# Kernel optimization log

Measured on AMD Instinct MI355X. Metric: run time of the kernel, lower is better.

Reference implementation:

```python
import jax, jax.numpy as jnp
import numpy as np

N, E, IN, H, L, G, C = 100000, 600000, 64, 128, 3, 256, 10
EPS_BN = 1e-5


def _tconv(x, src, dst, Wq, bq, Wk, bk, Wv, bv, Ws, bs):
    # PyG TransformerConv, heads=1: per-edge dot-product attention softmaxed over
    # in-neighbors of each target node, plus root (skip) linear.
    n = x.shape[0]
    q = x @ Wq + bq                      # [N,H]
    k = x @ Wk + bk                      # [N,H]
    v = x @ Wv + bv                      # [N,H]
    scale = 1.0 / jnp.sqrt(jnp.asarray(q.shape[-1], x.dtype))
    a = jnp.sum(q[dst] * k[src], axis=-1) * scale          # [E]
    m = jax.ops.segment_max(a, dst, num_segments=n)         # per-target max
    ex = jnp.exp(a - m[dst])
    s = jax.ops.segment_sum(ex, dst, num_segments=n)
    w = ex / s[dst]                                          # softmax over edges per target
    agg = jax.ops.segment_sum(v[src] * w[:, None], dst, num_segments=n)  # [N,H]
    return agg + x @ Ws + bs


def _bn(x, g, b):
    # BatchNorm1d, training mode: biased batch variance, eps=1e-5
    mu = jnp.mean(x, axis=0)
    var = jnp.mean((x - mu) ** 2, axis=0)
    return (x - mu) * jax.lax.rsqrt(var + EPS_BN) * g + b


def setup_inputs():
    key = jax.random.key(0)
    ks = jax.random.split(key, 40)
    sc = 0.05
    inp = {
        "x": jax.random.normal(ks[0], (N, IN), dtype=jnp.float32),
        "edge_index": jax.random.randint(ks[1], (2, E), 0, N, dtype=jnp.int32),
        "batch": jnp.sort(jax.random.randint(ks[2], (N,), 0, G, dtype=jnp.int32)),
        # conv1: input_dim -> hidden
        "Wq1": jax.random.normal(ks[3], (IN, H)) * sc,
        "bq1": jnp.zeros((H,), jnp.float32),
        "Wk1": jax.random.normal(ks[4], (IN, H)) * sc,
        "bk1": jnp.zeros((H,), jnp.float32),
        "Wv1": jax.random.normal(ks[5], (IN, H)) * sc,
        "bv1": jnp.zeros((H,), jnp.float32),
        "Ws1": jax.random.normal(ks[6], (IN, H)) * sc,
        "bs1": jnp.zeros((H,), jnp.float32),
        "bn1_g": jnp.ones((H,), jnp.float32),
        "bn1_b": jnp.zeros((H,), jnp.float32),
        # stacked hidden layers: hidden -> hidden
        "Wq": jax.random.normal(ks[7], (L, H, H)) * sc,
        "bq": jnp.zeros((L, H), jnp.float32),
        "Wk": jax.random.normal(ks[8], (L, H, H)) * sc,
        "bk": jnp.zeros((L, H), jnp.float32),
        "Wv": jax.random.normal(ks[9], (L, H, H)) * sc,
        "bv": jnp.zeros((L, H), jnp.float32),
        "Ws": jax.random.normal(ks[10], (L, H, H)) * sc,
        "bs": jnp.zeros((L, H), jnp.float32),
        "bn_g": jnp.ones((L, H), jnp.float32),
        "bn_b": jnp.zeros((L, H), jnp.float32),
        # classifier head
        "lin_W": jax.random.normal(ks[11], (H, C)) * sc,
        "lin_b": jnp.zeros((C,), jnp.float32),
    }
    return inp


def reference(x, edge_index, batch, Wq1, bq1, Wk1, bk1, Wv1, bv1, Ws1, bs1,
              bn1_g, bn1_b, Wq, bq, Wk, bk, Wv, bv, Ws, bs, bn_g, bn_b,
              lin_W, lin_b):
    src, dst = edge_index[0], edge_index[1]
    h = _tconv(x, src, dst, Wq1, bq1, Wk1, bk1, Wv1, bv1, Ws1, bs1)
    h = jax.nn.relu(_bn(h, bn1_g, bn1_b))
    for i in range(L):
        h = _tconv(h, src, dst, Wq[i], bq[i], Wk[i], bk[i], Wv[i], bv[i], Ws[i], bs[i])
        h = jax.nn.relu(_bn(h, bn_g[i], bn_b[i]))
    # global_mean_pool over graphs
    sums = jax.ops.segment_sum(h, batch, num_segments=G)          # [G,H]
    cnts = jax.ops.segment_sum(jnp.ones((h.shape[0],), h.dtype), batch, num_segments=G)
    pooled = sums / jnp.maximum(cnts, 1.0)[:, None]
    return pooled @ lin_W + lin_b                                  # [G,C]
```

## Files before the change

kernel.cpp:

```cpp
#include <hip/hip_runtime.h>
#include <hip/hip_bf16.h>

#define IN_DIM 64
#define H_DIM 128
#define L_LAYERS 3
#define G_GRAPHS 256
#define C_CLASSES 10

typedef short bf16x8 __attribute__((ext_vector_type(8)));
typedef float f32x4 __attribute__((ext_vector_type(4)));

__device__ inline unsigned short bf16rne(float x) {
    unsigned v = __float_as_uint(x);
    v += 0x7FFFu + ((v >> 16) & 1u);
    return (unsigned short)(v >> 16);
}

__device__ inline void bsplit(float x, unsigned short& h, unsigned short& l) {
    h = bf16rne(x);
    float hf = __uint_as_float((unsigned)h << 16);
    l = bf16rne(x - hf);
}

__global__ void count_deg(const int* __restrict__ dst, int* __restrict__ deg,
                          int* __restrict__ erank, int e) {
    int i = blockIdx.x * blockDim.x + threadIdx.x;
    if (i < e) erank[i] = atomicAdd(&deg[dst[i]], 1);
}

__global__ __launch_bounds__(256) void scan1(const int* __restrict__ deg,
                                             int* __restrict__ rowptr,
                                             int* __restrict__ bsum, int n) {
    int i = blockIdx.x * 256 + threadIdx.x;
    int v = (i < n) ? deg[i] : 0;
    __shared__ int sm[256];
    sm[threadIdx.x] = v;
    __syncthreads();
    for (int off = 1; off < 256; off <<= 1) {
        int x = (threadIdx.x >= off) ? sm[threadIdx.x - off] : 0;
        __syncthreads();
        sm[threadIdx.x] += x;
        __syncthreads();
    }
    if (i < n) rowptr[i + 1] = sm[threadIdx.x];
    if (threadIdx.x == 255) bsum[blockIdx.x] = sm[255];
}

__global__ __launch_bounds__(512) void scan2(int* __restrict__ bsum, int nblk) {
    __shared__ int sm[512];
    int t = threadIdx.x;
    int v = (t < nblk) ? bsum[t] : 0;
    sm[t] = v;
    __syncthreads();
    for (int off = 1; off < 512; off <<= 1) {
        int x = (t >= off) ? sm[t - off] : 0;
        __syncthreads();
        sm[t] += x;
        __syncthreads();
    }
    if (t < nblk) bsum[t] = sm[t] - v;
}

__global__ void scan3(int* __restrict__ rowptr, const int* __restrict__ bsum, int n) {
    int i = blockIdx.x * 256 + threadIdx.x;
    if (i < n) rowptr[i + 1] += bsum[i >> 8];
    if (i == 0) rowptr[0] = 0;
}

__global__ void scatter_edges(const int* __restrict__ src, const int* __restrict__ dst,
                              const int* __restrict__ rowptr, const int* __restrict__ erank,
                              int* __restrict__ esrc, int e) {
    int i = blockIdx.x * blockDim.x + threadIdx.x;
    if (i < e) esrc[rowptr[dst[i]] + erank[i]] = src[i];
}

template <int K, bool BN>
__global__ __launch_bounds__(256) void prep_x(const float* __restrict__ X, int nrows,
                                              int rows_pad,
                                              const float* __restrict__ bnsc,
                                              const float* __restrict__ bnsh,
                                              unsigned short* __restrict__ XF) {
    const int GPR = K / 8;
    int e8 = blockIdx.x * 256 + threadIdx.x;
    int row = e8 / GPR;
    int k0 = (e8 - row * GPR) * 8;
    if (row >= rows_pad) return;
    float v[8];
    if (row < nrows) {
        float4 a = *(const float4*)(X + (size_t)row * K + k0);
        float4 b = *(const float4*)(X + (size_t)row * K + k0 + 4);
        v[0] = a.x; v[1] = a.y; v[2] = a.z; v[3] = a.w;
        v[4] = b.x; v[5] = b.y; v[6] = b.z; v[7] = b.w;
        if (BN) {
            float4 s0 = *(const float4*)(bnsc + k0);
            float4 s1 = *(const float4*)(bnsc + k0 + 4);
            float4 h0 = *(const float4*)(bnsh + k0);
            float4 h1 = *(const float4*)(bnsh + k0 + 4);
            v[0] = fmaxf(0.f, fmaf(v[0], s0.x, h0.x));
            v[1] = fmaxf(0.f, fmaf(v[1], s0.y, h0.y));
            v[2] = fmaxf(0.f, fmaf(v[2], s0.z, h0.z));
            v[3] = fmaxf(0.f, fmaf(v[3], s0.w, h0.w));
            v[4] = fmaxf(0.f, fmaf(v[4], s1.x, h1.x));
            v[5] = fmaxf(0.f, fmaf(v[5], s1.y, h1.y));
            v[6] = fmaxf(0.f, fmaf(v[6], s1.z, h1.z));
            v[7] = fmaxf(0.f, fmaf(v[7], s1.w, h1.w));
        }
    } else {
#pragma unroll
        for (int j = 0; j < 8; ++j) v[j] = 0.f;
    }
    unsigned short h[8], l[8];
#pragma unroll
    for (int j = 0; j < 8; ++j) bsplit(v[j], h[j], l[j]);
    size_t f = (size_t)(row >> 4) * (K >> 5) + (k0 >> 5);
    int lane = ((k0 >> 3) & 3) * 16 + (row & 15);
    unsigned short* p = XF + f * 1024 + lane * 8;
    uint4 hv, lv;
    hv.x = h[0] | (h[1] << 16); hv.y = h[2] | (h[3] << 16);
    hv.z = h[4] | (h[5] << 16); hv.w = h[6] | (h[7] << 16);
    lv.x = l[0] | (l[1] << 16); lv.y = l[2] | (l[3] << 16);
    lv.z = l[4] | (l[5] << 16); lv.w = l[6] | (l[7] << 16);
    *(uint4*)p = hv;
    *(uint4*)(p + 512) = lv;
}

template <int K>
__global__ __launch_bounds__(256) void prep_w(const float* __restrict__ W0,
                                              const float* __restrict__ W1,
                                              const float* __restrict__ W2,
                                              const float* __restrict__ W3,
                                              unsigned short* __restrict__ WF) {
    const float* W;
    switch (blockIdx.y) {
        case 0:  W = W0; break;
        case 1:  W = W1; break;
        case 2:  W = W2; break;
        default: W = W3; break;
    }
    const int GPC = K / 8;
    int e8 = blockIdx.x * 256 + threadIdx.x;
    if (e8 >= K * 16) return;
    int col = e8 / GPC;
    int k0 = (e8 - col * GPC) * 8;
    float v[8];
#pragma unroll
    for (int j = 0; j < 8; ++j) v[j] = W[(size_t)(k0 + j) * 128 + col];
    unsigned short h[8], l[8];
#pragma unroll
    for (int j = 0; j < 8; ++j) bsplit(v[j], h[j], l[j]);
    size_t f = (size_t)(col >> 4) * (K >> 5) + (k0 >> 5);
    int lane = ((k0 >> 3) & 3) * 16 + (col & 15);
    const size_t wstride = (size_t)8 * (K >> 5) * 1024;
    unsigned short* p = WF + blockIdx.y * wstride + f * 1024 + lane * 8;
    uint4 hv, lv;
    hv.x = h[0] | (h[1] << 16); hv.y = h[2] | (h[3] << 16);
    hv.z = h[4] | (h[5] << 16); hv.w = h[6] | (h[7] << 16);
    lv.x = l[0] | (l[1] << 16); lv.y = l[2] | (l[3] << 16);
    lv.z = l[4] | (l[5] << 16); lv.w = l[6] | (l[7] << 16);
    *(uint4*)p = hv;
    *(uint4*)(p + 512) = lv;
}

template <int K>
__global__ __launch_bounds__(256) void gemm_mfma(
    const unsigned short* __restrict__ XF, const unsigned short* __restrict__ WF,
    int n, int strips,
    const float* __restrict__ b0, const float* __restrict__ b1,
    const float* __restrict__ b2, const float* __restrict__ b3,
    float* __restrict__ oq, unsigned short* __restrict__ ok,
    unsigned short* __restrict__ ov, float* __restrict__ oskip) {
    constexpr int KB = K >> 5;
    int wid = (blockIdx.x * 256 + threadIdx.x) >> 6;
    int l = threadIdx.x & 63;
    if (wid >= strips) return;

    bf16x8 A[2][KB][2];
#pragma unroll
    for (int mf = 0; mf < 2; ++mf)
#pragma unroll
        for (int kb = 0; kb < KB; ++kb) {
            const unsigned short* p =
                XF + ((size_t)(wid * 2 + mf) * KB + kb) * 1024 + l * 8;
            A[mf][kb][0] = *(const bf16x8*)p;
            A[mf][kb][1] = *(const bf16x8*)(p + 512);
        }

    const int rbase = wid * 32 + ((l >> 4) << 2);
#pragma unroll
    for (int nf = 0; nf < 8; ++nf) {
        const int col = nf * 16 + (l & 15);
#pragma unroll
        for (int y = 0; y < 4; ++y) {
            const float* bias = (y == 0) ? b0 : (y == 1) ? b1 : (y == 2) ? b2 : b3;
            const unsigned short* WFy = WF + (size_t)y * (8 * KB * 1024);
            bf16x8 B[KB][2];
#pragma unroll
            for (int kb = 0; kb < KB; ++kb) {
                const unsigned short* p = WFy + ((size_t)(nf * KB + kb)) * 1024 + l * 8;
                B[kb][0] = *(const bf16x8*)p;
                B[kb][1] = *(const bf16x8*)(p + 512);
            }
            f32x4 acc[2];
            acc[0] = (f32x4){0.f, 0.f, 0.f, 0.f};
            acc[1] = (f32x4){0.f, 0.f, 0.f, 0.f};
#pragma unroll
            for (int kb = 0; kb < KB; ++kb) {
#pragma unroll
                for (int mf = 0; mf < 2; ++mf) {
                    acc[mf] = __builtin_amdgcn_mfma_f32_16x16x32_bf16(
                        A[mf][kb][0], B[kb][0], acc[mf], 0, 0, 0);
                    acc[mf] = __builtin_amdgcn_mfma_f32_16x16x32_bf16(
                        A[mf][kb][0], B[kb][1], acc[mf], 0, 0, 0);
                    acc[mf] = __builtin_amdgcn_mfma_f32_16x16x32_bf16(
                        A[mf][kb][1], B[kb][0], acc[mf], 0, 0, 0);
                }
            }
            float bb = bias[col];
            if (y == 0 || y == 3) {
                float* outp = (y == 0) ? oq : oskip;
#pragma unroll
                for (int mf = 0; mf < 2; ++mf)
#pragma unroll
                    for (int r = 0; r < 4; ++r) {
                        int row = rbase + mf * 16 + r;
                        if (row < n) outp[(size_t)row * 128 + col] = acc[mf][r] + bb;
                    }
            } else {
                unsigned short* outp = (y == 1) ? ok : ov;
#pragma unroll
                for (int mf = 0; mf < 2; ++mf)
#pragma unroll
                    for (int r = 0; r < 4; ++r) {
                        int row = rbase + mf * 16 + r;
                        if (row < n) outp[(size_t)row * 128 + col] = bf16rne(acc[mf][r] + bb);
                    }
            }
        }
    }
}

__global__ __launch_bounds__(256) void attn_kernel(
    const float* __restrict__ q, const unsigned short* __restrict__ k16,
    const unsigned short* __restrict__ v16,
    const int* __restrict__ rowptr, const int* __restrict__ esrc,
    float* __restrict__ h2, int n) {
    int wid = (blockIdx.x * blockDim.x + threadIdx.x) >> 6;
    int lane = threadIdx.x & 63;
    if (wid >= n) return;
    int f0 = lane * 2;
    float2 qv = *(const float2*)(q + (size_t)wid * 128 + f0);
    const float scale = 0.08838834764831845f;
    int beg = rowptr[wid], end = rowptr[wid + 1];
    if (beg == end) return;
    float m = -3.402823466e38f, ssum = 0.f, acc0 = 0.f, acc1 = 0.f;

    unsigned kA[4], vA[4];
#pragma unroll
    for (int c = 0; c < 4; ++c) {
        int jj = beg + c; jj = jj < end ? jj : end - 1;
        int s = esrc[jj];
        kA[c] = *(const unsigned*)(k16 + (size_t)s * 128 + f0);
        vA[c] = *(const unsigned*)(v16 + (size_t)s * 128 + f0);
    }
    for (int j = beg; j < end; j += 4) {
        unsigned kB[4], vB[4];
        if (j + 4 < end) {
#pragma unroll
            for (int c = 0; c < 4; ++c) {
                int jj = j + 4 + c; jj = jj < end ? jj : end - 1;
                int s = esrc[jj];
                kB[c] = *(const unsigned*)(k16 + (size_t)s * 128 + f0);
                vB[c] = *(const unsigned*)(v16 + (size_t)s * 128 + f0);
            }
        } else {
#pragma unroll
            for (int c = 0; c < 4; ++c) { kB[c] = 0; vB[c] = 0; }
        }
        int cnt = end - j;
#pragma unroll
        for (int c = 0; c < 4; ++c) {
            if (c < cnt) {
                unsigned kw = kA[c], vw = vA[c];
                float kx = __uint_as_float(kw << 16);
                float ky = __uint_as_float(kw & 0xFFFF0000u);
                float d = qv.x * kx + qv.y * ky;
#pragma unroll
                for (int off = 32; off; off >>= 1) d += __shfl_xor(d, off);
                d *= scale;
                if (d > m) {
                    float r = __expf(m - d);
                    ssum *= r; acc0 *= r; acc1 *= r; m = d;
                }
                float w = __expf(d - m);
                ssum += w;
                acc0 += w * __uint_as_float(vw << 16);
                acc1 += w * __uint_as_float(vw & 0xFFFF0000u);
            }
        }
#pragma unroll
        for (int c = 0; c < 4; ++c) { kA[c] = kB[c]; vA[c] = vB[c]; }
    }
    float inv = 1.f / ssum;
    float2* o = (float2*)(h2 + (size_t)wid * 128 + f0);
    float2 cur = *o;
    cur.x += acc0 * inv;
    cur.y += acc1 * inv;
    *o = cur;
}

__global__ __launch_bounds__(256) void bn_stats(const float* __restrict__ h2,
                                                float* __restrict__ psum,
                                                float* __restrict__ psq, int n) {
    int f = threadIdx.x & 127;
    int rp = threadIdx.x >> 7;
    float s = 0.f, s2 = 0.f;
    for (int r = blockIdx.x * 2 + rp; r < n; r += gridDim.x * 2) {
        float x = h2[(size_t)r * 128 + f];
        s += x;
        s2 += x * x;
    }
    __shared__ float sm[256], sm2[256];
    sm[threadIdx.x] = s;
    sm2[threadIdx.x] = s2;
    __syncthreads();
    if (rp == 0) {
        psum[blockIdx.x * 128 + f] = sm[f] + sm[128 + f];
        psq[blockIdx.x * 128 + f] = sm2[f] + sm2[128 + f];
    }
}

__global__ __launch_bounds__(512) void bn_finalize(const float* __restrict__ psum,
                                                   const float* __restrict__ psq,
                                                   const float* __restrict__ g,
                                                   const float* __restrict__ b,
                                                   float* __restrict__ scale,
                                                   float* __restrict__ shift, int n) {
    int f = threadIdx.x & 127, part = threadIdx.x >> 7;
    float s = 0.f, s2 = 0.f;
#pragma unroll 4
    for (int i = part; i < 256; i += 4) {
        s += psum[i * 128 + f];
        s2 += psq[i * 128 + f];
    }
    __shared__ float sa[512], sb[512];
    sa[threadIdx.x] = s;
    sb[threadIdx.x] = s2;
    __syncthreads();
    if (part == 0) {
        s = sa[f] + sa[128 + f] + sa[256 + f] + sa[384 + f];
        s2 = sb[f] + sb[128 + f] + sb[256 + f] + sb[384 + f];
        float inv_n = 1.f / (float)n;
        float mu = s * inv_n;
        float var = s2 * inv_n - mu * mu;
        float sc = g[f] * rsqrtf(var + 1e-5f);
        scale[f] = sc;
        shift[f] = b[f] - mu * sc;
    }
}

__global__ __launch_bounds__(256) void pool_kernel(const float* __restrict__ h,
                                                   const float* __restrict__ bnsc,
                                                   const float* __restrict__ bnsh,
                                                   const int* __restrict__ batch,
                                                   float* __restrict__ pooled, int n) {
    int g = blockIdx.x;
    int lo = 0, hi = n;
    while (lo < hi) { int mid = (lo + hi) >> 1; if (batch[mid] < g) lo = mid + 1; else hi = mid; }
    int start = lo;
    lo = start; hi = n;
    while (lo < hi) { int mid = (lo + hi) >> 1; if (batch[mid] < g + 1) lo = mid + 1; else hi = mid; }
    int end = lo;
    int f = threadIdx.x & 127, rp = threadIdx.x >> 7;
    float sc = bnsc[f], sh = bnsh[f];
    float s = 0.f;
    for (int r = start + rp; r < end; r += 2)
        s += fmaxf(0.f, fmaf(h[(size_t)r * 128 + f], sc, sh));
    __shared__ float sm[256];
    sm[threadIdx.x] = s;
    __syncthreads();
    if (rp == 0) {
        float tot = sm[f] + sm[128 + f];
        float cnt = (float)(end - start);
        pooled[g * 128 + f] = tot / fmaxf(cnt, 1.f);
    }
}

__global__ void head_kernel(const float* __restrict__ pooled, const float* __restrict__ W,
                            const float* __restrict__ bias, float* __restrict__ out) {
    int g = blockIdx.x;
    int lane = threadIdx.x;
    float p0 = pooled[g * 128 + lane];
    float p1 = pooled[g * 128 + 64 + lane];
#pragma unroll
    for (int c = 0; c < C_CLASSES; ++c) {
        float d = p0 * W[lane * C_CLASSES + c] + p1 * W[(64 + lane) * C_CLASSES + c];
#pragma unroll
        for (int off = 32; off; off >>= 1) d += __shfl_xor(d, off);
        if (lane == 0) out[g * C_CLASSES + c] = d + bias[c];
    }
}

extern "C" void kernel_launch(void* const* d_in, const int* in_sizes, int n_in,
                              void* d_out, int out_size, void* d_ws, size_t ws_size,
                              hipStream_t stream) {
    const int N = in_sizes[0] / IN_DIM;
    const int E = in_sizes[1] / 2;

    const float* x     = (const float*)d_in[0];
    const int* ei      = (const int*)d_in[1];
    const int* src     = ei;
    const int* dst     = ei + E;
    const int* batch   = (const int*)d_in[2];
    const float* Wq1 = (const float*)d_in[3],  *bq1 = (const float*)d_in[4];
    const float* Wk1 = (const float*)d_in[5],  *bk1 = (const float*)d_in[6];
    const float* Wv1 = (const float*)d_in[7],  *bv1 = (const float*)d_in[8];
    const float* Ws1 = (const float*)d_in[9],  *bs1 = (const float*)d_in[10];
    const float* bn1g = (const float*)d_in[11], *bn1b = (const float*)d_in[12];
    const float* Wq = (const float*)d_in[13], *bq = (const float*)d_in[14];
    const float* Wk = (const float*)d_in[15], *bk = (const float*)d_in[16];
    const float* Wv = (const float*)d_in[17], *bv = (const float*)d_in[18];
    const float* Ws = (const float*)d_in[19], *bs = (const float*)d_in[20];
    const float* bng = (const float*)d_in[21], *bnb = (const float*)d_in[22];
    const float* linW = (const float*)d_in[23], *linb = (const float*)d_in[24];
    float* out = (float*)d_out;

    const int RB = (N + 127) / 128;
    const int rows_pad = RB * 128;
    const int strips = rows_pad / 32;

    char* w = (char*)d_ws;
    auto alloc = [&](size_t bytes) -> char* {
        char* p = w;
        w += (bytes + 255) & ~(size_t)255;
        return p;
    };
    const size_t NH = (size_t)N * H_DIM;
    float* q    = (float*)alloc(NH * 4);
    float* conv = (float*)alloc(NH * 4);
    unsigned short* k16 = (unsigned short*)alloc(NH * 2);
    unsigned short* v16 = (unsigned short*)alloc(NH * 2);
    unsigned short* XF = (unsigned short*)alloc((size_t)rows_pad * H_DIM * 2 * 2);
    unsigned short* WF = (unsigned short*)alloc((size_t)4 * H_DIM * H_DIM * 2 * 2);
    float* psum = (float*)alloc(256 * 128 * 4);
    float* psq  = (float*)alloc(256 * 128 * 4);
    float* bnsc = (float*)alloc(128 * 4);
    float* bnsh = (float*)alloc(128 * 4);
    float* pooled = (float*)alloc(G_GRAPHS * H_DIM * 4);
    int* deg    = (int*)alloc((size_t)N * 4);
    int* rowptr = (int*)alloc((size_t)(N + 1) * 4);
    int* erank  = (int*)alloc((size_t)E * 4);
    int* esrc   = (int*)alloc((size_t)E * 4);
    int* bsum   = (int*)alloc(((size_t)(N + 255) / 256) * 4);

    const int nblk = (N + 255) / 256;
    const int egrid = (E + 255) / 256;

    hipMemsetAsync(deg, 0, (size_t)N * 4, stream);
    count_deg<<<egrid, 256, 0, stream>>>(dst, deg, erank, E);
    scan1<<<nblk, 256, 0, stream>>>(deg, rowptr, bsum, N);
    scan2<<<1, 512, 0, stream>>>(bsum, nblk);
    scan3<<<nblk, 256, 0, stream>>>(rowptr, bsum, N);
    scatter_edges<<<egrid, 256, 0, stream>>>(src, dst, rowptr, erank, esrc, E);

    const int attn_blocks = (N + 3) / 4;
    const int gemm_blocks = (strips + 3) / 4;

    {
        const int px_grid = rows_pad * IN_DIM / 8 / 256;
        prep_x<IN_DIM, false><<<px_grid, 256, 0, stream>>>(x, N, rows_pad, nullptr, nullptr, XF);
        prep_w<IN_DIM><<<dim3((IN_DIM * 16 + 255) / 256, 4), 256, 0, stream>>>(Wq1, Wk1, Wv1, Ws1, WF);
        gemm_mfma<IN_DIM><<<gemm_blocks, 256, 0, stream>>>(
            XF, WF, N, strips, bq1, bk1, bv1, bs1, q, k16, v16, conv);
        attn_kernel<<<attn_blocks, 256, 0, stream>>>(q, k16, v16, rowptr, esrc, conv, N);
        bn_stats<<<256, 256, 0, stream>>>(conv, psum, psq, N);
        bn_finalize<<<1, 512, 0, stream>>>(psum, psq, bn1g, bn1b, bnsc, bnsh, N);
    }

    for (int i = 0; i < L_LAYERS; ++i) {
        const size_t wo = (size_t)i * H_DIM * H_DIM;
        const size_t bo = (size_t)i * H_DIM;
        const int px_grid = rows_pad * H_DIM / 8 / 256;
        prep_x<H_DIM, true><<<px_grid, 256, 0, stream>>>(conv, N, rows_pad, bnsc, bnsh, XF);
        prep_w<H_DIM><<<dim3((H_DIM * 16 + 255) / 256, 4), 256, 0, stream>>>(
            Wq + wo, Wk + wo, Wv + wo, Ws + wo, WF);
        gemm_mfma<H_DIM><<<gemm_blocks, 256, 0, stream>>>(
            XF, WF, N, strips, bq + bo, bk + bo, bv + bo, bs + bo, q, k16, v16, conv);
        attn_kernel<<<attn_blocks, 256, 0, stream>>>(q, k16, v16, rowptr, esrc, conv, N);
        bn_stats<<<256, 256, 0, stream>>>(conv, psum, psq, N);
        bn_finalize<<<1, 512, 0, stream>>>(psum, psq, bng + bo, bnb + bo, bnsc, bnsh, N);
    }

    pool_kernel<<<G_GRAPHS, 256, 0, stream>>>(conv, bnsc, bnsh, batch, pooled, N);
    head_kernel<<<G_GRAPHS, 64, 0, stream>>>(pooled, linW, linb, out);
}
```

Before: 1.129 ms.

## Fuse input prep into GEMM, interleave K/V, and process two edges per wave

Removes the separate prep_x pass by loading fp32 activations, applying BN+ReLU and bf16 hi/lo splitting inside the GEMM, using ping-pong conv buffers so the input is not overwritten. All layer weights are pre-split once up front instead of per layer. K and V are stored interleaved per row so one gather fetches both, and the attention kernel splits each wave into two half-waves that process alternate edges with wider per-lane loads, merging the online-softmax states at the end. This cuts an intermediate write/read per layer and halves shuffle depth per edge, at the cost of redundant conversion work in the GEMM and a more complex attention merge.

```diff
diff --git a/kernel.cpp b/kernel.cpp
--- a/kernel.cpp
+++ b/kernel.cpp
@@ -74,47 +74,22 @@
     if (i < e) esrc[rowptr[dst[i]] + erank[i]] = src[i];
 }
 
-template <int K, bool BN>
-__global__ __launch_bounds__(256) void prep_x(const float* __restrict__ X, int nrows,
-                                              int rows_pad,
-                                              const float* __restrict__ bnsc,
-                                              const float* __restrict__ bnsh,
-                                              unsigned short* __restrict__ XF) {
-    const int GPR = K / 8;
-    int e8 = blockIdx.x * 256 + threadIdx.x;
-    int row = e8 / GPR;
-    int k0 = (e8 - row * GPR) * 8;
-    if (row >= rows_pad) return;
+template <int K>
+__device__ inline void prep_w_one(const float* __restrict__ W,
+                                  unsigned short* __restrict__ WFm, int e8) {
+    const int GPC = K / 8;
+    if (e8 >= K * 16) return;
+    int col = e8 / GPC;
+    int k0 = (e8 - col * GPC) * 8;
     float v[8];
-    if (row < nrows) {
-        float4 a = *(const float4*)(X + (size_t)row * K + k0);
-        float4 b = *(const float4*)(X + (size_t)row * K + k0 + 4);
-        v[0] = a.x; v[1] = a.y; v[2] = a.z; v[3] = a.w;
-        v[4] = b.x; v[5] = b.y; v[6] = b.z; v[7] = b.w;
-        if (BN) {
-            float4 s0 = *(const float4*)(bnsc + k0);
-            float4 s1 = *(const float4*)(bnsc + k0 + 4);
-            float4 h0 = *(const float4*)(bnsh + k0);
-            float4 h1 = *(const float4*)(bnsh + k0 + 4);
-            v[0] = fmaxf(0.f, fmaf(v[0], s0.x, h0.x));
-            v[1] = fmaxf(0.f, fmaf(v[1], s0.y, h0.y));
-            v[2] = fmaxf(0.f, fmaf(v[2], s0.z, h0.z));
-            v[3] = fmaxf(0.f, fmaf(v[3], s0.w, h0.w));
-            v[4] = fmaxf(0.f, fmaf(v[4], s1.x, h1.x));
-            v[5] = fmaxf(0.f, fmaf(v[5], s1.y, h1.y));
-            v[6] = fmaxf(0.f, fmaf(v[6], s1.z, h1.z));
-            v[7] = fmaxf(0.f, fmaf(v[7], s1.w, h1.w));
-        }
-    } else {
-#pragma unroll
-        for (int j = 0; j < 8; ++j) v[j] = 0.f;
-    }
+#pragma unroll
+    for (int j = 0; j < 8; ++j) v[j] = W[(size_t)(k0 + j) * 128 + col];
     unsigned short h[8], l[8];
 #pragma unroll
     for (int j = 0; j < 8; ++j) bsplit(v[j], h[j], l[j]);
-    size_t f = (size_t)(row >> 4) * (K >> 5) + (k0 >> 5);
-    int lane = ((k0 >> 3) & 3) * 16 + (row & 15);
-    unsigned short* p = XF + f * 1024 + lane * 8;
+    size_t f = (size_t)(col >> 4) * (K >> 5) + (k0 >> 5);
+    int lane = ((k0 >> 3) & 3) * 16 + (col & 15);
+    unsigned short* p = WFm + f * 1024 + lane * 8;
     uint4 hv, lv;
     hv.x = h[0] | (h[1] << 16); hv.y = h[2] | (h[3] << 16);
     hv.z = h[4] | (h[5] << 16); hv.w = h[6] | (h[7] << 16);
@@ -124,66 +99,78 @@
     *(uint4*)(p + 512) = lv;
 }
 
-template <int K>
-__global__ __launch_bounds__(256) void prep_w(const float* __restrict__ W0,
-                                              const float* __restrict__ W1,
-                                              const float* __restrict__ W2,
-                                              const float* __restrict__ W3,
-                                              unsigned short* __restrict__ WF) {
-    const float* W;
-    switch (blockIdx.y) {
-        case 0:  W = W0; break;
-        case 1:  W = W1; break;
-        case 2:  W = W2; break;
-        default: W = W3; break;
-    }
-    const int GPC = K / 8;
-    int e8 = blockIdx.x * 256 + threadIdx.x;
-    if (e8 >= K * 16) return;
-    int col = e8 / GPC;
-    int k0 = (e8 - col * GPC) * 8;
-    float v[8];
-#pragma unroll
-    for (int j = 0; j < 8; ++j) v[j] = W[(size_t)(k0 + j) * 128 + col];
-    unsigned short h[8], l[8];
-#pragma unroll
-    for (int j = 0; j < 8; ++j) bsplit(v[j], h[j], l[j]);
-    size_t f = (size_t)(col >> 4) * (K >> 5) + (k0 >> 5);
-    int lane = ((k0 >> 3) & 3) * 16 + (col & 15);
-    const size_t wstride = (size_t)8 * (K >> 5) * 1024;
-    unsigned short* p = WF + blockIdx.y * wstride + f * 1024 + lane * 8;
-    uint4 hv, lv;
-    hv.x = h[0] | (h[1] << 16); hv.y = h[2] | (h[3] << 16);
-    hv.z = h[4] | (h[5] << 16); hv.w = h[6] | (h[7] << 16);
-    lv.x = l[0] | (l[1] << 16); lv.y = l[2] | (l[3] << 16);
-    lv.z = l[4] | (l[5] << 16); lv.w = l[6] | (l[7] << 16);
-    *(uint4*)p = hv;
-    *(uint4*)(p + 512) = lv;
-}
-
-template <int K>
-__global__ __launch_bounds__(256) void gemm_mfma(
-    const unsigned short* __restrict__ XF, const unsigned short* __restrict__ WF,
+__global__ __launch_bounds__(256) void prep_w64(const float* __restrict__ W0,
+                                                const float* __restrict__ W1,
+                                                const float* __restrict__ W2,
+                                                const float* __restrict__ W3,
+                                                unsigned short* __restrict__ WF) {
+    const float* W = (blockIdx.y == 0) ? W0 : (blockIdx.y == 1) ? W1
+                   : (blockIdx.y == 2) ? W2 : W3;
+    prep_w_one<IN_DIM>(W, WF + (size_t)blockIdx.y * 16384,
+                       blockIdx.x * 256 + threadIdx.x);
+}
+
+__global__ __launch_bounds__(256) void prep_w128(const float* __restrict__ Wq,
+                                                 const float* __restrict__ Wk,
+                                                 const float* __restrict__ Wv,
+                                                 const float* __restrict__ Ws,
+                                                 unsigned short* __restrict__ WF) {
+    int layer = blockIdx.y >> 2, mat = blockIdx.y & 3;
+    const float* base = (mat == 0) ? Wq : (mat == 1) ? Wk : (mat == 2) ? Wv : Ws;
+    const float* W = base + (size_t)layer * H_DIM * H_DIM;
+    unsigned short* o = WF + 65536 + (size_t)blockIdx.y * 32768;
+    prep_w_one<H_DIM>(W, o, blockIdx.x * 256 + threadIdx.x);
+}
+
+template <int K, bool BN>
+__global__ __launch_bounds__(256) void gemm_fused(
+    const float* __restrict__ X, const unsigned short* __restrict__ WF,
     int n, int strips,
+    const float* __restrict__ bnsc, const float* __restrict__ bnsh,
     const float* __restrict__ b0, const float* __restrict__ b1,
     const float* __restrict__ b2, const float* __restrict__ b3,
-    float* __restrict__ oq, unsigned short* __restrict__ ok,
-    unsigned short* __restrict__ ov, float* __restrict__ oskip) {
+    float* __restrict__ oq, unsigned short* __restrict__ okv,
+    float* __restrict__ oskip) {
     constexpr int KB = K >> 5;
     int wid = (blockIdx.x * 256 + threadIdx.x) >> 6;
     int l = threadIdx.x & 63;
     if (wid >= strips) return;
+    const int r16 = l & 15;
+    const int ko8 = (l >> 4) * 8;
 
     bf16x8 A[2][KB][2];
 #pragma unroll
-    for (int mf = 0; mf < 2; ++mf)
-#pragma unroll
-        for (int kb = 0; kb < KB; ++kb) {
-            const unsigned short* p =
-                XF + ((size_t)(wid * 2 + mf) * KB + kb) * 1024 + l * 8;
-            A[mf][kb][0] = *(const bf16x8*)p;
-            A[mf][kb][1] = *(const bf16x8*)(p + 512);
+    for (int kb = 0; kb < KB; ++kb) {
+        float sc[8], sh[8];
+        if (BN) {
+            *(float4*)sc       = *(const float4*)(bnsc + kb * 32 + ko8);
+            *(float4*)(sc + 4) = *(const float4*)(bnsc + kb * 32 + ko8 + 4);
+            *(float4*)sh       = *(const float4*)(bnsh + kb * 32 + ko8);
+            *(float4*)(sh + 4) = *(const float4*)(bnsh + kb * 32 + ko8 + 4);
         }
+#pragma unroll
+        for (int mf = 0; mf < 2; ++mf) {
+            int row = wid * 32 + mf * 16 + r16;
+            int rowc = row < n ? row : n - 1;
+            const float* px = X + (size_t)rowc * K + kb * 32 + ko8;
+            float v[8];
+            *(float4*)v       = *(const float4*)px;
+            *(float4*)(v + 4) = *(const float4*)(px + 4);
+            if (BN) {
+#pragma unroll
+                for (int j = 0; j < 8; ++j) v[j] = fmaxf(0.f, fmaf(v[j], sc[j], sh[j]));
+            }
+            bf16x8 hi, lo;
+#pragma unroll
+            for (int j = 0; j < 8; ++j) {
+                unsigned short h, l2;
+                bsplit(v[j], h, l2);
+                hi[j] = (short)h; lo[j] = (short)l2;
+            }
+            A[mf][kb][0] = hi;
+            A[mf][kb][1] = lo;
+        }
+    }
 
     const int rbase = wid * 32 + ((l >> 4) << 2);
 #pragma unroll
@@ -226,13 +213,14 @@
                         if (row < n) outp[(size_t)row * 128 + col] = acc[mf][r] + bb;
                     }
             } else {
-                unsigned short* outp = (y == 1) ? ok : ov;
+                const int voff = (y == 2) ? 128 : 0;
 #pragma unroll
                 for (int mf = 0; mf < 2; ++mf)
 #pragma unroll
                     for (int r = 0; r < 4; ++r) {
                         int row = rbase + mf * 16 + r;
-                        if (row < n) outp[(size_t)row * 128 + col] = bf16rne(acc[mf][r] + bb);
+                        if (row < n)
+                            okv[(size_t)row * 256 + voff + col] = bf16rne(acc[mf][r] + bb);
                     }
             }
         }
@@ -240,72 +228,94 @@
 }
 
 __global__ __launch_bounds__(256) void attn_kernel(
-    const float* __restrict__ q, const unsigned short* __restrict__ k16,
-    const unsigned short* __restrict__ v16,
+    const float* __restrict__ q, const unsigned short* __restrict__ kv,
     const int* __restrict__ rowptr, const int* __restrict__ esrc,
     float* __restrict__ h2, int n) {
     int wid = (blockIdx.x * blockDim.x + threadIdx.x) >> 6;
     int lane = threadIdx.x & 63;
     if (wid >= n) return;
-    int f0 = lane * 2;
-    float2 qv = *(const float2*)(q + (size_t)wid * 128 + f0);
+    const int g = lane >> 5;
+    const int f0 = (lane & 31) * 4;
+    float4 qv = *(const float4*)(q + (size_t)wid * 128 + f0);
     const float scale = 0.08838834764831845f;
     int beg = rowptr[wid], end = rowptr[wid + 1];
     if (beg == end) return;
-    float m = -3.402823466e38f, ssum = 0.f, acc0 = 0.f, acc1 = 0.f;
-
-    unsigned kA[4], vA[4];
-#pragma unroll
-    for (int c = 0; c < 4; ++c) {
-        int jj = beg + c; jj = jj < end ? jj : end - 1;
-        int s = esrc[jj];
-        kA[c] = *(const unsigned*)(k16 + (size_t)s * 128 + f0);
-        vA[c] = *(const unsigned*)(v16 + (size_t)s * 128 + f0);
-    }
-    for (int j = beg; j < end; j += 4) {
-        unsigned kB[4], vB[4];
-        if (j + 4 < end) {
-#pragma unroll
-            for (int c = 0; c < 4; ++c) {
-                int jj = j + 4 + c; jj = jj < end ? jj : end - 1;
-                int s = esrc[jj];
-                kB[c] = *(const unsigned*)(k16 + (size_t)s * 128 + f0);
-                vB[c] = *(const unsigned*)(v16 + (size_t)s * 128 + f0);
-            }
-        } else {
-#pragma unroll
-            for (int c = 0; c < 4; ++c) { kB[c] = 0; vB[c] = 0; }
+    float m = -3.402823466e38f, ssum = 0.f;
+    float a0 = 0.f, a1 = 0.f, a2 = 0.f, a3 = 0.f;
+
+#define FETCH(J, KU, VU) {                                                   \
+        int jj = (J) + g;                                                    \
+        if (jj < end) {                                                      \
+            int s = esrc[jj];                                                \
+            const unsigned short* p = kv + (size_t)s * 256 + f0;             \
+            KU = *(const uint2*)p;                                           \
+            VU = *(const uint2*)(p + 128);                                   \
+        } else { KU.x = 0u; KU.y = 0u; VU.x = 0u; VU.y = 0u; } }
+
+#define PROC(J, KU, VU) {                                                    \
+        float kx0 = __uint_as_float(KU.x << 16);                             \
+        float kx1 = __uint_as_float(KU.x & 0xFFFF0000u);                     \
+        float kx2 = __uint_as_float(KU.y << 16);                             \
+        float kx3 = __uint_as_float(KU.y & 0xFFFF0000u);                     \
+        float d = qv.x * kx0 + qv.y * kx1 + qv.z * kx2 + qv.w * kx3;         \
+        d += __shfl_xor(d, 1);  d += __shfl_xor(d, 2);  d += __shfl_xor(d, 4); \
+        d += __shfl_xor(d, 8);  d += __shfl_xor(d, 16);                      \
+        d *= scale;                                                          \
+        if ((J) + g < end) {                                                 \
+            if (d > m) {                                                     \
+                float r = __expf(m - d);                                     \
+                ssum *= r; a0 *= r; a1 *= r; a2 *= r; a3 *= r; m = d;        \
+            }                                                                \
+            float w = __expf(d - m);                                         \
+            ssum += w;                                                       \
+            a0 += w * __uint_as_float(VU.x << 16);                           \
+            a1 += w * __uint_as_float(VU.x & 0xFFFF0000u);                   \
+            a2 += w * __uint_as_float(VU.y << 16);                           \
+            a3 += w * __uint_as_float(VU.y & 0xFFFF0000u);                   \
+        } }
+
+    uint2 kA, vA, kB, vB;
+    FETCH(beg, kA, vA);
+    FETCH(beg + 2, kB, vB);
+    int j = beg;
+    for (;;) {
+        {
+            uint2 kN, vN;
+            FETCH(j + 4, kN, vN);
+            PROC(j, kA, vA);
+            kA = kN; vA = vN;
         }
-        int cnt = end - j;
-#pragma unroll
-        for (int c = 0; c < 4; ++c) {
-            if (c < cnt) {
-                unsigned kw = kA[c], vw = vA[c];
-                float kx = __uint_as_float(kw << 16);
-                float ky = __uint_as_float(kw & 0xFFFF0000u);
-                float d = qv.x * kx + qv.y * ky;
-#pragma unroll
-                for (int off = 32; off; off >>= 1) d += __shfl_xor(d, off);
-                d *= scale;
-                if (d > m) {
-                    float r = __expf(m - d);
-                    ssum *= r; acc0 *= r; acc1 *= r; m = d;
-                }
-                float w = __expf(d - m);
-                ssum += w;
-                acc0 += w * __uint_as_float(vw << 16);
-                acc1 += w * __uint_as_float(vw & 0xFFFF0000u);
-            }
+        j += 2; if (j >= end) break;
+        {
+            uint2 kN, vN;
+            FETCH(j + 4, kN, vN);
+            PROC(j, kB, vB);
+            kB = kN; vB = vN;
         }
-#pragma unroll
-        for (int c = 0; c < 4; ++c) { kA[c] = kB[c]; vA[c] = vB[c]; }
-    }
-    float inv = 1.f / ssum;
-    float2* o = (float2*)(h2 + (size_t)wid * 128 + f0);
-    float2 cur = *o;
-    cur.x += acc0 * inv;
-    cur.y += acc1 * inv;
-    *o = cur;
+        j += 2; if (j >= end) break;
+    }
+#undef FETCH
+#undef PROC
+
+    float mo = __shfl_xor(m, 32);
+    float m2 = fmaxf(m, mo);
+    float fac = __expf(m - m2);
+    ssum *= fac; a0 *= fac; a1 *= fac; a2 *= fac; a3 *= fac;
+    ssum += __shfl_xor(ssum, 32);
+    a0 += __shfl_xor(a0, 32);
+    a1 += __shfl_xor(a1, 32);
+    a2 += __shfl_xor(a2, 32);
+    a3 += __shfl_xor(a3, 32);
+    if (lane < 32) {
+        float inv = 1.f / ssum;
+        float4* o = (float4*)(h2 + (size_t)wid * 128 + f0);
+        float4 cur = *o;
+        cur.x += a0 * inv;
+        cur.y += a1 * inv;
+        cur.z += a2 * inv;
+        cur.w += a3 * inv;
+        *o = cur;
+    }
 }
 
 __global__ __launch_bounds__(256) void bn_stats(const float* __restrict__ h2,
@@ -424,9 +434,7 @@
     const float* linW = (const float*)d_in[23], *linb = (const float*)d_in[24];
     float* out = (float*)d_out;
 
-    const int RB = (N + 127) / 128;
-    const int rows_pad = RB * 128;
-    const int strips = rows_pad / 32;
+    const int strips = (N + 31) / 32;
 
     char* w = (char*)d_ws;
     auto alloc = [&](size_t bytes) -> char* {
@@ -435,12 +443,11 @@
         return p;
     };
     const size_t NH = (size_t)N * H_DIM;
-    float* q    = (float*)alloc(NH * 4);
-    float* conv = (float*)alloc(NH * 4);
-    unsigned short* k16 = (unsigned short*)alloc(NH * 2);
-    unsigned short* v16 = (unsigned short*)alloc(NH * 2);
-    unsigned short* XF = (unsigned short*)alloc((size_t)rows_pad * H_DIM * 2 * 2);
-    unsigned short* WF = (unsigned short*)alloc((size_t)4 * H_DIM * H_DIM * 2 * 2);
+    float* q     = (float*)alloc(NH * 4);
+    float* convA = (float*)alloc(NH * 4);
+    float* convB = (float*)alloc(NH * 4);
+    unsigned short* kv16 = (unsigned short*)alloc((size_t)N * 256 * 2);
+    unsigned short* WF   = (unsigned short*)alloc((size_t)(65536 + 12 * 32768) * 2);
     float* psum = (float*)alloc(256 * 128 * 4);
     float* psq  = (float*)alloc(256 * 128 * 4);
     float* bnsc = (float*)alloc(128 * 4);
@@ -457,6 +464,8 @@
 
     hipMemsetAsync(deg, 0, (size_t)N * 4, stream);
     count_deg<<<egrid, 256, 0, stream>>>(dst, deg, erank, E);
+    prep_w64<<<dim3(4, 4), 256, 0, stream>>>(Wq1, Wk1, Wv1, Ws1, WF);
+    prep_w128<<<dim3(8, 12), 256, 0, stream>>>(Wq, Wk, Wv, Ws, WF);
     scan1<<<nblk, 256, 0, stream>>>(deg, rowptr, bsum, N);
     scan2<<<1, 512, 0, stream>>>(bsum, nblk);
     scan3<<<nblk, 256, 0, stream>>>(rowptr, bsum, N);
@@ -465,31 +474,26 @@
     const int attn_blocks = (N + 3) / 4;
     const int gemm_blocks = (strips + 3) / 4;
 
-    {
-        const int px_grid = rows_pad * IN_DIM / 8 / 256;
-        prep_x<IN_DIM, false><<<px_grid, 256, 0, stream>>>(x, N, rows_pad, nullptr, nullptr, XF);
-        prep_w<IN_DIM><<<dim3((IN_DIM * 16 + 255) / 256, 4), 256, 0, stream>>>(Wq1, Wk1, Wv1, Ws1, WF);
-        gemm_mfma<IN_DIM><<<gemm_blocks, 256, 0, stream>>>(
-            XF, WF, N, strips, bq1, bk1, bv1, bs1, q, k16, v16, conv);
-        attn_kernel<<<attn_blocks, 256, 0, stream>>>(q, k16, v16, rowptr, esrc, conv, N);
-        bn_stats<<<256, 256, 0, stream>>>(conv, psum, psq, N);
-        bn_finalize<<<1, 512, 0, stream>>>(psum, psq, bn1g, bn1b, bnsc, bnsh, N);
-    }
-
+    gemm_fused<IN_DIM, false><<<gemm_blocks, 256, 0, stream>>>(
+        x, WF, N, strips, nullptr, nullptr, bq1, bk1, bv1, bs1, q, kv16, convA);
+    attn_kernel<<<attn_blocks, 256, 0, stream>>>(q, kv16, rowptr, esrc, convA, N);
+    bn_stats<<<256, 256, 0, stream>>>(convA, psum, psq, N);
+    bn_finalize<<<1, 512, 0, stream>>>(psum, psq, bn1g, bn1b, bnsc, bnsh, N);
+
+    float* cur = convA;
+    float* nxt = convB;
     for (int i = 0; i < L_LAYERS; ++i) {
-        const size_t wo = (size_t)i * H_DIM * H_DIM;
         const size_t bo = (size_t)i * H_DIM;
-        const int px_grid = rows_pad * H_DIM / 8 / 256;
-        prep_x<H_DIM, true><<<px_grid, 256, 0, stream>>>(conv, N, rows_pad, bnsc, bnsh, XF);
-        prep_w<H_DIM><<<dim3((H_DIM * 16 + 255) / 256, 4), 256, 0, stream>>>(
-            Wq + wo, Wk + wo, Wv + wo, Ws + wo, WF);
-        gemm_mfma<H_DIM><<<gemm_blocks, 256, 0, stream>>>(
-            XF, WF, N, strips, bq + bo, bk + bo, bv + bo, bs + bo, q, k16, v16, conv);
-        attn_kernel<<<attn_blocks, 256, 0, stream>>>(q, k16, v16, rowptr, esrc, conv, N);
-        bn_stats<<<256, 256, 0, stream>>>(conv, psum, psq, N);
+        const unsigned short* WFl = WF + 65536 + (size_t)i * 4 * 32768;
+        gemm_fused<H_DIM, true><<<gemm_blocks, 256, 0, stream>>>(
+            cur, WFl, N, strips, bnsc, bnsh, bq + bo, bk + bo, bv + bo, bs + bo,
+            q, kv16, nxt);
+        attn_kernel<<<attn_blocks, 256, 0, stream>>>(q, kv16, rowptr, esrc, nxt, N);
+        bn_stats<<<256, 256, 0, stream>>>(nxt, psum, psq, N);
         bn_finalize<<<1, 512, 0, stream>>>(psum, psq, bng + bo, bnb + bo, bnsc, bnsh, N);
-    }
-
-    pool_kernel<<<G_GRAPHS, 256, 0, stream>>>(conv, bnsc, bnsh, batch, pooled, N);
+        float* t = cur; cur = nxt; nxt = t;
+    }
+
+    pool_kernel<<<G_GRAPHS, 256, 0, stream>>>(cur, bnsc, bnsh, batch, pooled, N);
     head_kernel<<<G_GRAPHS, 64, 0, stream>>>(pooled, linW, linb, out);
 }
```

After: 1.039 ms. -8.0%, faster.
